# Performance work log

Measured on AMD Instinct MI355X. Metric: run time of the kernel, lower is better.

Reference implementation:

```python
import jax, jax.numpy as jnp
import numpy as np


def setup_inputs() -> dict:
    key = jax.random.key(0)
    ks = jax.random.split(key, 6)
    Q, S, D, C = 128, 512, 768, 64
    return {
        "query_reps": jax.random.normal(ks[0], (Q, D), dtype=jnp.float32),
        "support_reps": jax.random.normal(ks[1], (S, D), dtype=jnp.float32),
        "W1": jax.random.normal(ks[2], (2 * D, 2 * D), dtype=jnp.float32) * 0.02,
        "b1": jnp.zeros((2 * D,), dtype=jnp.float32),
        "W2": jax.random.normal(ks[3], (1, 2 * D), dtype=jnp.float32) * 0.02,
        "b2": jnp.zeros((1,), dtype=jnp.float32),
        "support_labels": jnp.sort(jax.random.randint(ks[4], (S,), 0, C)),
        "query_target_ids": jax.random.randint(ks[5], (Q,), 0, C),
        "num_classes": C,
    }


def reference(query_reps, support_reps, W1, b1, W2, b2,
              support_labels, query_target_ids, num_classes):
    D = query_reps.shape[1]
    # Original: concat_reps = cat([repeat_interleave(q, S), s.repeat(Q)], dim=1)
    # then relu(Linear_2Dx2D(concat)). Equivalent split-weight form avoids the
    # explicit [Q*S, 2D] concat: x @ W1.T = q @ W1[:, :D].T + s @ W1[:, D:].T
    hq = query_reps @ W1[:, :D].T        # [Q, 2D]
    hs = support_reps @ W1[:, D:].T      # [S, 2D]
    h = jax.nn.relu(hq[:, None, :] + hs[None, :, :] + b1)   # [Q, S, 2D]
    scores = jnp.einsum('qsd,d->qs', h, W2[0]) + b2[0]       # [Q, S]
    # aggregate_scores_by_label with support_reduction='score':
    # M one-hot [C, S] row-normalized (p=1) => per-label mean of scores.
    seg = jax.ops.segment_sum(scores.T, support_labels,
                              num_segments=num_classes).T     # [Q, C]
    counts = jax.ops.segment_sum(jnp.ones((support_labels.shape[0],), jnp.float32),
                                 support_labels, num_segments=num_classes)
    agg = seg / jnp.maximum(counts, 1.0)                      # [Q, C]
    logp = jax.nn.log_softmax(agg, axis=1)
    loss = -jnp.mean(jnp.take_along_axis(logp, query_target_ids[:, None], axis=1))
    preds = jnp.argmax(agg, axis=1)
    return (loss, preds == query_target_ids)
```

## Files before the change

### kernel.cpp

```cpp
#include <hip/hip_runtime.h>
#include <math.h>

#define QN 128
#define SN 512
#define DN 768
#define TDN 1536
#define CN 64
#define KSPLIT 4
#define KCH 192

#define HQP_ELEMS (KSPLIT * QN * TDN)
#define HSP_ELEMS (KSPLIT * SN * TDN)
#define ZERO_ELEMS (QN * CN)

typedef short short8 __attribute__((ext_vector_type(8)));
typedef float f32x4 __attribute__((ext_vector_type(4)));

#define LDS_STRIDE 40
#define PLANE (128 * LDS_STRIDE)

__device__ __forceinline__ short bf16_rtn(float x) {
    unsigned u = __float_as_uint(x);
    return (short)((u + 0x7fffu + ((u >> 16) & 1u)) >> 16);
}
__device__ __forceinline__ float bf16_tof(short s) {
    return __uint_as_float(((unsigned)(unsigned short)s) << 16);
}

__global__ __launch_bounds__(256) void gemm_kernel(
    const float* __restrict__ query, const float* __restrict__ support,
    const float* __restrict__ W1, float* __restrict__ hqp, float* __restrict__ hsp,
    float* __restrict__ zbuf, float* __restrict__ out)
{
    const int nt = blockIdx.x;
    const int mt = blockIdx.y;
    const int kz = blockIdx.z;
    const int tid = threadIdx.x;

    if (nt == 0 && kz == 0) {
        int o = (mt * 256 + tid) * 8;
        if (o < ZERO_ELEMS) {
            *(float4*)&zbuf[o]     = make_float4(0.f, 0.f, 0.f, 0.f);
            *(float4*)&zbuf[o + 4] = make_float4(0.f, 0.f, 0.f, 0.f);
        }
        if (mt == 0 && tid == 0) out[0] = 0.0f;
    }

    const float* A;
    float* Cout;
    int M0, Koff;
    if (mt == 0) { A = query;   M0 = 0;              Koff = 0;  Cout = hqp + (size_t)kz * QN * TDN; }
    else         { A = support; M0 = (mt - 1) * 128; Koff = DN; Cout = hsp + (size_t)kz * SN * TDN; }

    __shared__ short lds[2][4][PLANE];

    const int r  = tid >> 1;
    const int kh = (tid & 1) * 16;

    const float* Arow = &A [(size_t)(M0 + r) * DN  + kz * KCH + kh];
    const float* Brow = &W1[(size_t)(nt * 128 + r) * TDN + Koff + kz * KCH + kh];

    f32x4 acc[4][4];
    #pragma unroll
    for (int i = 0; i < 4; ++i)
        #pragma unroll
        for (int j = 0; j < 4; ++j)
            acc[i][j] = (f32x4){0.f, 0.f, 0.f, 0.f};

    auto stage = [&](short* plane, float4 v0, float4 v1, float4 v2, float4 v3) {
        float f[16] = {v0.x,v0.y,v0.z,v0.w, v1.x,v1.y,v1.z,v1.w,
                       v2.x,v2.y,v2.z,v2.w, v3.x,v3.y,v3.z,v3.w};
        short hi[16], lo[16];
        #pragma unroll
        for (int i = 0; i < 16; ++i) {
            hi[i] = bf16_rtn(f[i]);
            lo[i] = bf16_rtn(f[i] - bf16_tof(hi[i]));
        }
        short* dsth = plane + r * LDS_STRIDE + kh;
        #pragma unroll
        for (int i = 0; i < 16; ++i) dsth[i] = hi[i];
        short* dstl = plane + PLANE + r * LDS_STRIDE + kh;
        #pragma unroll
        for (int i = 0; i < 16; ++i) dstl[i] = lo[i];
    };

    {
        float4 a0 = *(const float4*)(Arow),     a1 = *(const float4*)(Arow + 4);
        float4 a2 = *(const float4*)(Arow + 8), a3 = *(const float4*)(Arow + 12);
        float4 b0 = *(const float4*)(Brow),     b1 = *(const float4*)(Brow + 4);
        float4 b2 = *(const float4*)(Brow + 8), b3 = *(const float4*)(Brow + 12);
        stage(lds[0][0], a0, a1, a2, a3);
        stage(lds[0][2], b0, b1, b2, b3);
    }
    __syncthreads();

    const int lane  = tid & 63;
    const int w     = tid >> 6;
    const int lm    = lane & 15;
    const int quad  = lane >> 4;
    const int wrow0 = (w >> 1) * 64;
    const int wcol0 = (w & 1) * 64;

    int buf = 0;
    for (int step = 0; step < 6; ++step) {
        float4 a0, a1, a2, a3, b0, b1, b2, b3;
        if (step < 5) {
            const float* An = Arow + (step + 1) * 32;
            const float* Bn = Brow + (step + 1) * 32;
            a0 = *(const float4*)(An);     a1 = *(const float4*)(An + 4);
            a2 = *(const float4*)(An + 8); a3 = *(const float4*)(An + 12);
            b0 = *(const float4*)(Bn);     b1 = *(const float4*)(Bn + 4);
            b2 = *(const float4*)(Bn + 8); b3 = *(const float4*)(Bn + 12);
        }

        const short* Ah = lds[buf][0];
        const short* Al = lds[buf][1];
        const short* Bh = lds[buf][2];
        const short* Bl = lds[buf][3];

        short8 ah[4], al[4], bh[4], bl[4];
        #pragma unroll
        for (int mi = 0; mi < 4; ++mi) {
            int off = (wrow0 + mi * 16 + lm) * LDS_STRIDE + quad * 8;
            ah[mi] = *(const short8*)&Ah[off];
            al[mi] = *(const short8*)&Al[off];
        }
        #pragma unroll
        for (int ni = 0; ni < 4; ++ni) {
            int off = (wcol0 + ni * 16 + lm) * LDS_STRIDE + quad * 8;
            bh[ni] = *(const short8*)&Bh[off];
            bl[ni] = *(const short8*)&Bl[off];
        }
        #pragma unroll
        for (int mi = 0; mi < 4; ++mi)
            #pragma unroll
            for (int ni = 0; ni < 4; ++ni) {
                acc[mi][ni] = __builtin_amdgcn_mfma_f32_16x16x32_bf16(ah[mi], bh[ni], acc[mi][ni], 0, 0, 0);
                acc[mi][ni] = __builtin_amdgcn_mfma_f32_16x16x32_bf16(ah[mi], bl[ni], acc[mi][ni], 0, 0, 0);
                acc[mi][ni] = __builtin_amdgcn_mfma_f32_16x16x32_bf16(al[mi], bh[ni], acc[mi][ni], 0, 0, 0);
            }

        if (step < 5) {
            int nb = buf ^ 1;
            stage(lds[nb][0], a0, a1, a2, a3);
            stage(lds[nb][2], b0, b1, b2, b3);
            __syncthreads();
            buf = nb;
        }
    }

    #pragma unroll
    for (int mi = 0; mi < 4; ++mi)
        #pragma unroll
        for (int ni = 0; ni < 4; ++ni) {
            int grow = M0 + wrow0 + mi * 16 + quad * 4;
            int gcol = nt * 128 + wcol0 + ni * 16 + lm;
            #pragma unroll
            for (int rr = 0; rr < 4; ++rr)
                Cout[(size_t)(grow + rr) * TDN + gcol] = acc[mi][ni][rr];
        }
}

__global__ __launch_bounds__(256) void score_kernel(
    const float* __restrict__ hqp, const float* __restrict__ hsp,
    const float* __restrict__ b1, const float* __restrict__ W2,
    const int* __restrict__ labels, float* __restrict__ aggbuf)
{
    const int jc = blockIdx.x;
    const int qt = blockIdx.y;
    const int st = blockIdx.z;

    __shared__ float hqT[96][64];
    __shared__ float hsT[96][64];
    __shared__ float w2s[96];
    __shared__ float sc[64][68];
    __shared__ int   lab[64];

    const int tid = threadIdx.x;
    if (tid < 64) lab[tid] = labels[st * 64 + tid];

    #pragma unroll
    for (int l = 0; l < 6; ++l) {
        int idx  = tid + l * 256;
        int row  = idx / 24;
        int quad = idx - row * 24;
        int j    = jc * 96 + quad * 4;
        float4 hv = *(const float4*)&b1[j];
        float4 sv = make_float4(0.f, 0.f, 0.f, 0.f);
        #pragma unroll
        for (int p = 0; p < KSPLIT; ++p) {
            float4 h = *(const float4*)&hqp[(size_t)p * QN * TDN + (size_t)(qt * 64 + row) * TDN + j];
            float4 g = *(const float4*)&hsp[(size_t)p * SN * TDN + (size_t)(st * 64 + row) * TDN + j];
            hv.x += h.x; hv.y += h.y; hv.z += h.z; hv.w += h.w;
            sv.x += g.x; sv.y += g.y; sv.z += g.z; sv.w += g.w;
        }
        hqT[quad*4+0][row] = hv.x; hqT[quad*4+1][row] = hv.y;
        hqT[quad*4+2][row] = hv.z; hqT[quad*4+3][row] = hv.w;
        hsT[quad*4+0][row] = sv.x; hsT[quad*4+1][row] = sv.y;
        hsT[quad*4+2][row] = sv.z; hsT[quad*4+3][row] = sv.w;
    }
    if (tid < 24) {
        float4 w = *(const float4*)&W2[jc * 96 + tid * 4];
        w2s[tid*4+0] = w.x; w2s[tid*4+1] = w.y;
        w2s[tid*4+2] = w.z; w2s[tid*4+3] = w.w;
    }
    __syncthreads();

    const int tx = tid & 15;
    const int ty = tid >> 4;
    float acc[4][4];
    #pragma unroll
    for (int i = 0; i < 4; ++i)
        #pragma unroll
        for (int j = 0; j < 4; ++j) acc[i][j] = 0.0f;

    #pragma unroll 4
    for (int jj = 0; jj < 96; ++jj) {
        float4 a4 = *(const float4*)&hqT[jj][ty * 4];
        float4 b4 = *(const float4*)&hsT[jj][tx * 4];
        float w = w2s[jj];
        float a[4] = {a4.x, a4.y, a4.z, a4.w};
        float b[4] = {b4.x, b4.y, b4.z, b4.w};
        #pragma unroll
        for (int i = 0; i < 4; ++i)
            #pragma unroll
            for (int j = 0; j < 4; ++j)
                acc[i][j] += w * fmaxf(a[i] + b[j], 0.0f);
    }

    #pragma unroll
    for (int i = 0; i < 4; ++i)
        *(float4*)&sc[ty * 4 + i][tx * 4] =
            make_float4(acc[i][0], acc[i][1], acc[i][2], acc[i][3]);
    __syncthreads();

    {
        int row = tid >> 2;
        int seg = tid & 3;
        float* aggrow = aggbuf + (size_t)(qt * 64 + row) * CN;
        int   runc = lab[seg * 16];
        float runv = 0.0f;
        #pragma unroll
        for (int k = 0; k < 16; ++k) {
            int s = seg * 16 + k;
            int c = lab[s];
            if (c != runc) { atomicAdd(&aggrow[runc], runv); runv = 0.0f; runc = c; }
            runv += sc[row][s];
        }
        atomicAdd(&aggrow[runc], runv);
    }
}

__global__ __launch_bounds__(256) void finale_kernel(
    const float* __restrict__ aggbuf, const int* __restrict__ labels,
    const int* __restrict__ tgt, float* __restrict__ out)
{
    __shared__ float cnt[CN];
    const int tid = threadIdx.x;
    if (tid < CN) cnt[tid] = 0.0f;
    __syncthreads();
    atomicAdd(&cnt[labels[tid]],       1.0f);
    atomicAdd(&cnt[labels[tid + 256]], 1.0f);
    __syncthreads();

    const int lane = tid & 63;
    const int q    = blockIdx.x * 4 + (tid >> 6);

    float v = aggbuf[(size_t)q * CN + lane] / fmaxf(cnt[lane], 1.0f);
    float av = v; int am = lane;
    #pragma unroll
    for (int off = 1; off < 64; off <<= 1) {
        float ov = __shfl_xor(av, off);
        int   oi = __shfl_xor(am, off);
        if (ov > av || (ov == av && oi < am)) { av = ov; am = oi; }
    }
    float m = av;
    float e = expf(v - m);
    #pragma unroll
    for (int off = 1; off < 64; off <<= 1)
        e += __shfl_xor(e, off);
    int t = tgt[q];
    float vt = __shfl(v, t, 64);
    if (lane == 0) {
        out[1 + q] = (am == t) ? 1.0f : 0.0f;
        atomicAdd(&out[0], -(vt - m - logf(e)) / (float)QN);
    }
}

extern "C" void kernel_launch(void* const* d_in, const int* in_sizes, int n_in,
                              void* d_out, int out_size, void* d_ws, size_t ws_size,
                              hipStream_t stream) {
    const float* query   = (const float*)d_in[0];
    const float* support = (const float*)d_in[1];
    const float* W1      = (const float*)d_in[2];
    const float* b1      = (const float*)d_in[3];
    const float* W2      = (const float*)d_in[4];
    const int* labels = (const int*)d_in[6];
    const int* tgt    = (const int*)d_in[7];

    float* ws     = (float*)d_ws;
    float* hqp    = ws;
    float* hsp    = hqp + HQP_ELEMS;
    float* aggbuf = hsp + HSP_ELEMS;
    float* out    = (float*)d_out;

    hipLaunchKernelGGL(gemm_kernel, dim3(12, 5, 4), dim3(256), 0, stream,
                       query, support, W1, hqp, hsp, aggbuf, out);
    hipLaunchKernelGGL(score_kernel, dim3(16, 2, 8), dim3(256), 0, stream,
                       hqp, hsp, b1, W2, labels, aggbuf);
    hipLaunchKernelGGL(finale_kernel, dim3(32), dim3(256), 0, stream,
                       aggbuf, labels, tgt, out);
}
```

Baseline: 119.0 us.

## Fuse GEMM, scoring and finale into one cooperative kernel with grid syncs

Replaces the three kernel launches with a single cooperative kernel of 256 blocks. Blocks 0-239 run the split-K GEMM, block 240 zeroes the aggregation buffer, and the score stage and finale follow after grid-wide barriers. The finale now runs in one block, with one thread per query doing a serial loop over classes, and the loss is reduced without global atomics. The goal is to remove launch gaps between kernels, at the cost of grid-sync overhead, a serialized single-block finale and LDS shared through a union.

Measured after the change: 202.7 us. 1.7x slower.

```diff
diff --git a/kernel.cpp b/kernel.cpp
--- a/kernel.cpp
+++ b/kernel.cpp
@@ -1,5 +1,8 @@
 #include <hip/hip_runtime.h>
+#include <hip/hip_cooperative_groups.h>
 #include <math.h>
+
+namespace cg = cooperative_groups;
 
 #define QN 128
 #define SN 512
@@ -11,7 +14,6 @@
 
 #define HQP_ELEMS (KSPLIT * QN * TDN)
 #define HSP_ELEMS (KSPLIT * SN * TDN)
-#define ZERO_ELEMS (QN * CN)
 
 typedef short short8 __attribute__((ext_vector_type(8)));
 typedef float f32x4 __attribute__((ext_vector_type(4)));
@@ -27,263 +29,280 @@
     return __uint_as_float(((unsigned)(unsigned short)s) << 16);
 }
 
-__global__ __launch_bounds__(256) void gemm_kernel(
+__global__ __launch_bounds__(256) void mega_kernel(
     const float* __restrict__ query, const float* __restrict__ support,
-    const float* __restrict__ W1, float* __restrict__ hqp, float* __restrict__ hsp,
-    float* __restrict__ zbuf, float* __restrict__ out)
+    const float* __restrict__ W1, const float* __restrict__ b1,
+    const float* __restrict__ W2, const int* __restrict__ labels,
+    const int* __restrict__ tgt, float* __restrict__ hqp,
+    float* __restrict__ hsp, float* __restrict__ aggbuf,
+    float* __restrict__ out)
 {
-    const int nt = blockIdx.x;
-    const int mt = blockIdx.y;
-    const int kz = blockIdx.z;
+    const int bid = blockIdx.x;
     const int tid = threadIdx.x;
 
-    if (nt == 0 && kz == 0) {
-        int o = (mt * 256 + tid) * 8;
-        if (o < ZERO_ELEMS) {
-            *(float4*)&zbuf[o]     = make_float4(0.f, 0.f, 0.f, 0.f);
-            *(float4*)&zbuf[o + 4] = make_float4(0.f, 0.f, 0.f, 0.f);
-        }
-        if (mt == 0 && tid == 0) out[0] = 0.0f;
+    __shared__ union {
+        short g[2][4][PLANE];
+        struct {
+            float hqT[96][64];
+            float hsT[96][64];
+            float w2s[96];
+            float sc[64][68];
+            int   lab[64];
+            float cnt[64];
+            float red[4];
+        } s;
+    } sh;
+
+    cg::grid_group grid = cg::this_grid();
+
+    if (bid >= 240) {
+        if (bid == 240) {
+            #pragma unroll
+            for (int i = 0; i < 8; ++i)
+                *(float4*)&aggbuf[(tid * 8 + i * 2048)] = make_float4(0.f,0.f,0.f,0.f);
+        }
+    } else {
+        const int nt = bid % 12;
+        const int mt = (bid / 12) % 5;
+        const int kz = bid / 60;
+
+        const float* A;
+        float* Cout;
+        int M0, Koff;
+        if (mt == 0) { A = query;   M0 = 0;              Koff = 0;  Cout = hqp + (size_t)kz * QN * TDN; }
+        else         { A = support; M0 = (mt - 1) * 128; Koff = DN; Cout = hsp + (size_t)kz * SN * TDN; }
+
+        const int r  = tid >> 1;
+        const int kh = (tid & 1) * 16;
+
+        const float* Arow = &A [(size_t)(M0 + r) * DN  + kz * KCH + kh];
+        const float* Brow = &W1[(size_t)(nt * 128 + r) * TDN + Koff + kz * KCH + kh];
+
+        f32x4 acc[4][4];
+        #pragma unroll
+        for (int i = 0; i < 4; ++i)
+            #pragma unroll
+            for (int j = 0; j < 4; ++j)
+                acc[i][j] = (f32x4){0.f, 0.f, 0.f, 0.f};
+
+        auto stage = [&](short* plane, float4 v0, float4 v1, float4 v2, float4 v3) {
+            float f[16] = {v0.x,v0.y,v0.z,v0.w, v1.x,v1.y,v1.z,v1.w,
+                           v2.x,v2.y,v2.z,v2.w, v3.x,v3.y,v3.z,v3.w};
+            short hi[16], lo[16];
+            #pragma unroll
+            for (int i = 0; i < 16; ++i) {
+                hi[i] = bf16_rtn(f[i]);
+                lo[i] = bf16_rtn(f[i] - bf16_tof(hi[i]));
+            }
+            short* dsth = plane + r * LDS_STRIDE + kh;
+            #pragma unroll
+            for (int i = 0; i < 16; ++i) dsth[i] = hi[i];
+            short* dstl = plane + PLANE + r * LDS_STRIDE + kh;
+            #pragma unroll
+            for (int i = 0; i < 16; ++i) dstl[i] = lo[i];
+        };
+
+        {
+            float4 a0 = *(const float4*)(Arow),     a1 = *(const float4*)(Arow + 4);
+            float4 a2 = *(const float4*)(Arow + 8), a3 = *(const float4*)(Arow + 12);
+            float4 b0 = *(const float4*)(Brow),     b1 = *(const float4*)(Brow + 4);
+            float4 b2 = *(const float4*)(Brow + 8), b3 = *(const float4*)(Brow + 12);
+            stage(sh.g[0][0], a0, a1, a2, a3);
+            stage(sh.g[0][2], b0, b1, b2, b3);
+        }
+        __syncthreads();
+
+        const int lane  = tid & 63;
+        const int w     = tid >> 6;
+        const int lm    = lane & 15;
+        const int quad  = lane >> 4;
+        const int wrow0 = (w >> 1) * 64;
+        const int wcol0 = (w & 1) * 64;
+
+        int buf = 0;
+        for (int step = 0; step < 6; ++step) {
+            float4 a0, a1, a2, a3, b0, b1, b2, b3;
+            if (step < 5) {
+                const float* An = Arow + (step + 1) * 32;
+                const float* Bn = Brow + (step + 1) * 32;
+                a0 = *(const float4*)(An);     a1 = *(const float4*)(An + 4);
+                a2 = *(const float4*)(An + 8); a3 = *(const float4*)(An + 12);
+                b0 = *(const float4*)(Bn);     b1 = *(const float4*)(Bn + 4);
+                b2 = *(const float4*)(Bn + 8); b3 = *(const float4*)(Bn + 12);
+            }
+
+            const short* Ah = sh.g[buf][0];
+            const short* Al = sh.g[buf][1];
+            const short* Bh = sh.g[buf][2];
+            const short* Bl = sh.g[buf][3];
+
+            short8 ah[4], al[4], bh[4], bl[4];
+            #pragma unroll
+            for (int mi = 0; mi < 4; ++mi) {
+                int off = (wrow0 + mi * 16 + lm) * LDS_STRIDE + quad * 8;
+                ah[mi] = *(const short8*)&Ah[off];
+                al[mi] = *(const short8*)&Al[off];
+            }
+            #pragma unroll
+            for (int ni = 0; ni < 4; ++ni) {
+                int off = (wcol0 + ni * 16 + lm) * LDS_STRIDE + quad * 8;
+                bh[ni] = *(const short8*)&Bh[off];
+                bl[ni] = *(const short8*)&Bl[off];
+            }
+            #pragma unroll
+            for (int mi = 0; mi < 4; ++mi)
+                #pragma unroll
+                for (int ni = 0; ni < 4; ++ni) {
+                    acc[mi][ni] = __builtin_amdgcn_mfma_f32_16x16x32_bf16(ah[mi], bh[ni], acc[mi][ni], 0, 0, 0);
+                    acc[mi][ni] = __builtin_amdgcn_mfma_f32_16x16x32_bf16(ah[mi], bl[ni], acc[mi][ni], 0, 0, 0);
+                    acc[mi][ni] = __builtin_amdgcn_mfma_f32_16x16x32_bf16(al[mi], bh[ni], acc[mi][ni], 0, 0, 0);
+                }
+
+            if (step < 5) {
+                int nb = buf ^ 1;
+                stage(sh.g[nb][0], a0, a1, a2, a3);
+                stage(sh.g[nb][2], b0, b1, b2, b3);
+                __syncthreads();
+                buf = nb;
+            }
+        }
+
+        #pragma unroll
+        for (int mi = 0; mi < 4; ++mi)
+            #pragma unroll
+            for (int ni = 0; ni < 4; ++ni) {
+                int grow = M0 + wrow0 + mi * 16 + quad * 4;
+                int gcol = nt * 128 + wcol0 + ni * 16 + lm;
+                #pragma unroll
+                for (int rr = 0; rr < 4; ++rr)
+                    Cout[(size_t)(grow + rr) * TDN + gcol] = acc[mi][ni][rr];
+            }
     }
 
-    const float* A;
-    float* Cout;
-    int M0, Koff;
-    if (mt == 0) { A = query;   M0 = 0;              Koff = 0;  Cout = hqp + (size_t)kz * QN * TDN; }
-    else         { A = support; M0 = (mt - 1) * 128; Koff = DN; Cout = hsp + (size_t)kz * SN * TDN; }
-
-    __shared__ short lds[2][4][PLANE];
-
-    const int r  = tid >> 1;
-    const int kh = (tid & 1) * 16;
-
-    const float* Arow = &A [(size_t)(M0 + r) * DN  + kz * KCH + kh];
-    const float* Brow = &W1[(size_t)(nt * 128 + r) * TDN + Koff + kz * KCH + kh];
-
-    f32x4 acc[4][4];
-    #pragma unroll
-    for (int i = 0; i < 4; ++i)
-        #pragma unroll
-        for (int j = 0; j < 4; ++j)
-            acc[i][j] = (f32x4){0.f, 0.f, 0.f, 0.f};
-
-    auto stage = [&](short* plane, float4 v0, float4 v1, float4 v2, float4 v3) {
-        float f[16] = {v0.x,v0.y,v0.z,v0.w, v1.x,v1.y,v1.z,v1.w,
-                       v2.x,v2.y,v2.z,v2.w, v3.x,v3.y,v3.z,v3.w};
-        short hi[16], lo[16];
-        #pragma unroll
-        for (int i = 0; i < 16; ++i) {
-            hi[i] = bf16_rtn(f[i]);
-            lo[i] = bf16_rtn(f[i] - bf16_tof(hi[i]));
-        }
-        short* dsth = plane + r * LDS_STRIDE + kh;
-        #pragma unroll
-        for (int i = 0; i < 16; ++i) dsth[i] = hi[i];
-        short* dstl = plane + PLANE + r * LDS_STRIDE + kh;
-        #pragma unroll
-        for (int i = 0; i < 16; ++i) dstl[i] = lo[i];
-    };
+    grid.sync();
 
     {
-        float4 a0 = *(const float4*)(Arow),     a1 = *(const float4*)(Arow + 4);
-        float4 a2 = *(const float4*)(Arow + 8), a3 = *(const float4*)(Arow + 12);
-        float4 b0 = *(const float4*)(Brow),     b1 = *(const float4*)(Brow + 4);
-        float4 b2 = *(const float4*)(Brow + 8), b3 = *(const float4*)(Brow + 12);
-        stage(lds[0][0], a0, a1, a2, a3);
-        stage(lds[0][2], b0, b1, b2, b3);
+        const int jc = bid & 15;
+        const int qt = (bid >> 4) & 1;
+        const int st = bid >> 5;
+
+        if (tid < 64) sh.s.lab[tid] = labels[st * 64 + tid];
+
+        #pragma unroll
+        for (int l = 0; l < 6; ++l) {
+            int idx  = tid + l * 256;
+            int row  = idx / 24;
+            int quad = idx - row * 24;
+            int j    = jc * 96 + quad * 4;
+            float4 hv = *(const float4*)&b1[j];
+            float4 sv = make_float4(0.f, 0.f, 0.f, 0.f);
+            #pragma unroll
+            for (int p = 0; p < KSPLIT; ++p) {
+                float4 h = *(const float4*)&hqp[(size_t)p * QN * TDN + (size_t)(qt * 64 + row) * TDN + j];
+                float4 g = *(const float4*)&hsp[(size_t)p * SN * TDN + (size_t)(st * 64 + row) * TDN + j];
+                hv.x += h.x; hv.y += h.y; hv.z += h.z; hv.w += h.w;
+                sv.x += g.x; sv.y += g.y; sv.z += g.z; sv.w += g.w;
+            }
+            sh.s.hqT[quad*4+0][row] = hv.x; sh.s.hqT[quad*4+1][row] = hv.y;
+            sh.s.hqT[quad*4+2][row] = hv.z; sh.s.hqT[quad*4+3][row] = hv.w;
+            sh.s.hsT[quad*4+0][row] = sv.x; sh.s.hsT[quad*4+1][row] = sv.y;
+            sh.s.hsT[quad*4+2][row] = sv.z; sh.s.hsT[quad*4+3][row] = sv.w;
+        }
+        if (tid < 24) {
+            float4 wv = *(const float4*)&W2[jc * 96 + tid * 4];
+            sh.s.w2s[tid*4+0] = wv.x; sh.s.w2s[tid*4+1] = wv.y;
+            sh.s.w2s[tid*4+2] = wv.z; sh.s.w2s[tid*4+3] = wv.w;
+        }
+        __syncthreads();
+
+        const int tx = tid & 15;
+        const int ty = tid >> 4;
+        float acc[4][4];
+        #pragma unroll
+        for (int i = 0; i < 4; ++i)
+            #pragma unroll
+            for (int j = 0; j < 4; ++j) acc[i][j] = 0.0f;
+
+        #pragma unroll 4
+        for (int jj = 0; jj < 96; ++jj) {
+            float4 a4 = *(const float4*)&sh.s.hqT[jj][ty * 4];
+            float4 b4 = *(const float4*)&sh.s.hsT[jj][tx * 4];
+            float wv = sh.s.w2s[jj];
+            float a[4] = {a4.x, a4.y, a4.z, a4.w};
+            float b[4] = {b4.x, b4.y, b4.z, b4.w};
+            #pragma unroll
+            for (int i = 0; i < 4; ++i)
+                #pragma unroll
+                for (int j = 0; j < 4; ++j)
+                    acc[i][j] += wv * fmaxf(a[i] + b[j], 0.0f);
+        }
+
+        #pragma unroll
+        for (int i = 0; i < 4; ++i)
+            *(float4*)&sh.s.sc[ty * 4 + i][tx * 4] =
+                make_float4(acc[i][0], acc[i][1], acc[i][2], acc[i][3]);
+        __syncthreads();
+
+        {
+            int row = tid >> 2;
+            int seg = tid & 3;
+            float* aggrow = aggbuf + (size_t)(qt * 64 + row) * CN;
+            int   runc = sh.s.lab[seg * 16];
+            float runv = 0.0f;
+            #pragma unroll
+            for (int k = 0; k < 16; ++k) {
+                int s = seg * 16 + k;
+                int c = sh.s.lab[s];
+                if (c != runc) { atomicAdd(&aggrow[runc], runv); runv = 0.0f; runc = c; }
+                runv += sh.s.sc[row][s];
+            }
+            atomicAdd(&aggrow[runc], runv);
+        }
     }
-    __syncthreads();
-
-    const int lane  = tid & 63;
-    const int w     = tid >> 6;
-    const int lm    = lane & 15;
-    const int quad  = lane >> 4;
-    const int wrow0 = (w >> 1) * 64;
-    const int wcol0 = (w & 1) * 64;
-
-    int buf = 0;
-    for (int step = 0; step < 6; ++step) {
-        float4 a0, a1, a2, a3, b0, b1, b2, b3;
-        if (step < 5) {
-            const float* An = Arow + (step + 1) * 32;
-            const float* Bn = Brow + (step + 1) * 32;
-            a0 = *(const float4*)(An);     a1 = *(const float4*)(An + 4);
-            a2 = *(const float4*)(An + 8); a3 = *(const float4*)(An + 12);
-            b0 = *(const float4*)(Bn);     b1 = *(const float4*)(Bn + 4);
-            b2 = *(const float4*)(Bn + 8); b3 = *(const float4*)(Bn + 12);
-        }
-
-        const short* Ah = lds[buf][0];
-        const short* Al = lds[buf][1];
-        const short* Bh = lds[buf][2];
-        const short* Bl = lds[buf][3];
-
-        short8 ah[4], al[4], bh[4], bl[4];
-        #pragma unroll
-        for (int mi = 0; mi < 4; ++mi) {
-            int off = (wrow0 + mi * 16 + lm) * LDS_STRIDE + quad * 8;
-            ah[mi] = *(const short8*)&Ah[off];
-            al[mi] = *(const short8*)&Al[off];
-        }
-        #pragma unroll
-        for (int ni = 0; ni < 4; ++ni) {
-            int off = (wcol0 + ni * 16 + lm) * LDS_STRIDE + quad * 8;
-            bh[ni] = *(const short8*)&Bh[off];
-            bl[ni] = *(const short8*)&Bl[off];
-        }
-        #pragma unroll
-        for (int mi = 0; mi < 4; ++mi)
-            #pragma unroll
-            for (int ni = 0; ni < 4; ++ni) {
-                acc[mi][ni] = __builtin_amdgcn_mfma_f32_16x16x32_bf16(ah[mi], bh[ni], acc[mi][ni], 0, 0, 0);
-                acc[mi][ni] = __builtin_amdgcn_mfma_f32_16x16x32_bf16(ah[mi], bl[ni], acc[mi][ni], 0, 0, 0);
-                acc[mi][ni] = __builtin_amdgcn_mfma_f32_16x16x32_bf16(al[mi], bh[ni], acc[mi][ni], 0, 0, 0);
-            }
-
-        if (step < 5) {
-            int nb = buf ^ 1;
-            stage(lds[nb][0], a0, a1, a2, a3);
-            stage(lds[nb][2], b0, b1, b2, b3);
-            __syncthreads();
-            buf = nb;
-        }
-    }
-
-    #pragma unroll
-    for (int mi = 0; mi < 4; ++mi)
-        #pragma unroll
-        for (int ni = 0; ni < 4; ++ni) {
-            int grow = M0 + wrow0 + mi * 16 + quad * 4;
-            int gcol = nt * 128 + wcol0 + ni * 16 + lm;
-            #pragma unroll
-            for (int rr = 0; rr < 4; ++rr)
-                Cout[(size_t)(grow + rr) * TDN + gcol] = acc[mi][ni][rr];
-        }
-}
-
-__global__ __launch_bounds__(256) void score_kernel(
-    const float* __restrict__ hqp, const float* __restrict__ hsp,
-    const float* __restrict__ b1, const float* __restrict__ W2,
-    const int* __restrict__ labels, float* __restrict__ aggbuf)
-{
-    const int jc = blockIdx.x;
-    const int qt = blockIdx.y;
-    const int st = blockIdx.z;
-
-    __shared__ float hqT[96][64];
-    __shared__ float hsT[96][64];
-    __shared__ float w2s[96];
-    __shared__ float sc[64][68];
-    __shared__ int   lab[64];
-
-    const int tid = threadIdx.x;
-    if (tid < 64) lab[tid] = labels[st * 64 + tid];
-
-    #pragma unroll
-    for (int l = 0; l < 6; ++l) {
-        int idx  = tid + l * 256;
-        int row  = idx / 24;
-        int quad = idx - row * 24;
-        int j    = jc * 96 + quad * 4;
-        float4 hv = *(const float4*)&b1[j];
-        float4 sv = make_float4(0.f, 0.f, 0.f, 0.f);
-        #pragma unroll
-        for (int p = 0; p < KSPLIT; ++p) {
-            float4 h = *(const float4*)&hqp[(size_t)p * QN * TDN + (size_t)(qt * 64 + row) * TDN + j];
-            float4 g = *(const float4*)&hsp[(size_t)p * SN * TDN + (size_t)(st * 64 + row) * TDN + j];
-            hv.x += h.x; hv.y += h.y; hv.z += h.z; hv.w += h.w;
-            sv.x += g.x; sv.y += g.y; sv.z += g.z; sv.w += g.w;
-        }
-        hqT[quad*4+0][row] = hv.x; hqT[quad*4+1][row] = hv.y;
-        hqT[quad*4+2][row] = hv.z; hqT[quad*4+3][row] = hv.w;
-        hsT[quad*4+0][row] = sv.x; hsT[quad*4+1][row] = sv.y;
-        hsT[quad*4+2][row] = sv.z; hsT[quad*4+3][row] = sv.w;
-    }
-    if (tid < 24) {
-        float4 w = *(const float4*)&W2[jc * 96 + tid * 4];
-        w2s[tid*4+0] = w.x; w2s[tid*4+1] = w.y;
-        w2s[tid*4+2] = w.z; w2s[tid*4+3] = w.w;
-    }
-    __syncthreads();
-
-    const int tx = tid & 15;
-    const int ty = tid >> 4;
-    float acc[4][4];
-    #pragma unroll
-    for (int i = 0; i < 4; ++i)
-        #pragma unroll
-        for (int j = 0; j < 4; ++j) acc[i][j] = 0.0f;
-
-    #pragma unroll 4
-    for (int jj = 0; jj < 96; ++jj) {
-        float4 a4 = *(const float4*)&hqT[jj][ty * 4];
-        float4 b4 = *(const float4*)&hsT[jj][tx * 4];
-        float w = w2s[jj];
-        float a[4] = {a4.x, a4.y, a4.z, a4.w};
-        float b[4] = {b4.x, b4.y, b4.z, b4.w};
-        #pragma unroll
-        for (int i = 0; i < 4; ++i)
-            #pragma unroll
-            for (int j = 0; j < 4; ++j)
-                acc[i][j] += w * fmaxf(a[i] + b[j], 0.0f);
-    }
-
-    #pragma unroll
-    for (int i = 0; i < 4; ++i)
-        *(float4*)&sc[ty * 4 + i][tx * 4] =
-            make_float4(acc[i][0], acc[i][1], acc[i][2], acc[i][3]);
-    __syncthreads();
-
-    {
-        int row = tid >> 2;
-        int seg = tid & 3;
-        float* aggrow = aggbuf + (size_t)(qt * 64 + row) * CN;
-        int   runc = lab[seg * 16];
-        float runv = 0.0f;
-        #pragma unroll
-        for (int k = 0; k < 16; ++k) {
-            int s = seg * 16 + k;
-            int c = lab[s];
-            if (c != runc) { atomicAdd(&aggrow[runc], runv); runv = 0.0f; runc = c; }
-            runv += sc[row][s];
-        }
-        atomicAdd(&aggrow[runc], runv);
-    }
-}
-
-__global__ __launch_bounds__(256) void finale_kernel(
-    const float* __restrict__ aggbuf, const int* __restrict__ labels,
-    const int* __restrict__ tgt, float* __restrict__ out)
-{
-    __shared__ float cnt[CN];
-    const int tid = threadIdx.x;
-    if (tid < CN) cnt[tid] = 0.0f;
-    __syncthreads();
-    atomicAdd(&cnt[labels[tid]],       1.0f);
-    atomicAdd(&cnt[labels[tid + 256]], 1.0f);
-    __syncthreads();
-
-    const int lane = tid & 63;
-    const int q    = blockIdx.x * 4 + (tid >> 6);
-
-    float v = aggbuf[(size_t)q * CN + lane] / fmaxf(cnt[lane], 1.0f);
-    float av = v; int am = lane;
-    #pragma unroll
-    for (int off = 1; off < 64; off <<= 1) {
-        float ov = __shfl_xor(av, off);
-        int   oi = __shfl_xor(am, off);
-        if (ov > av || (ov == av && oi < am)) { av = ov; am = oi; }
-    }
-    float m = av;
-    float e = expf(v - m);
-    #pragma unroll
-    for (int off = 1; off < 64; off <<= 1)
-        e += __shfl_xor(e, off);
-    int t = tgt[q];
-    float vt = __shfl(v, t, 64);
-    if (lane == 0) {
-        out[1 + q] = (am == t) ? 1.0f : 0.0f;
-        atomicAdd(&out[0], -(vt - m - logf(e)) / (float)QN);
+
+    grid.sync();
+
+    if (bid == 0) {
+        if (tid < CN) sh.s.cnt[tid] = 0.0f;
+        __syncthreads();
+        atomicAdd(&sh.s.cnt[labels[tid]],       1.0f);
+        atomicAdd(&sh.s.cnt[labels[tid + 256]], 1.0f);
+        __syncthreads();
+
+        float lossv = 0.0f;
+        if (tid < QN) {
+            const int q = tid;
+            const float* rowp = aggbuf + (size_t)q * CN;
+            float v[CN];
+            #pragma unroll
+            for (int c4 = 0; c4 < 16; ++c4) {
+                float4 t4 = *(const float4*)&rowp[c4 * 4];
+                v[c4*4+0] = t4.x; v[c4*4+1] = t4.y;
+                v[c4*4+2] = t4.z; v[c4*4+3] = t4.w;
+            }
+            const int t = tgt[q];
+            float vt = 0.0f;
+            float best = -1e30f; int bi = 0;
+            #pragma unroll
+            for (int c = 0; c < CN; ++c) {
+                v[c] /= fmaxf(sh.s.cnt[c], 1.0f);
+                if (c == t) vt = v[c];
+                if (v[c] > best) { best = v[c]; bi = c; }
+            }
+            float e = 0.0f;
+            #pragma unroll
+            for (int c = 0; c < CN; ++c)
+                e += expf(v[c] - best);
+            out[1 + q] = (bi == t) ? 1.0f : 0.0f;
+            lossv = -(vt - best - logf(e));
+        }
+        #pragma unroll
+        for (int off = 1; off < 64; off <<= 1)
+            lossv += __shfl_xor(lossv, off);
+        if ((tid & 63) == 0) sh.s.red[tid >> 6] = lossv;
+        __syncthreads();
+        if (tid == 0)
+            out[0] = (sh.s.red[0] + sh.s.red[1]) / (float)QN;
     }
 }
 
@@ -304,10 +323,9 @@
     float* aggbuf = hsp + HSP_ELEMS;
     float* out    = (float*)d_out;
 
-    hipLaunchKernelGGL(gemm_kernel, dim3(12, 5, 4), dim3(256), 0, stream,
-                       query, support, W1, hqp, hsp, aggbuf, out);
-    hipLaunchKernelGGL(score_kernel, dim3(16, 2, 8), dim3(256), 0, stream,
-                       hqp, hsp, b1, W2, labels, aggbuf);
-    hipLaunchKernelGGL(finale_kernel, dim3(32), dim3(256), 0, stream,
-                       aggbuf, labels, tgt, out);
+    void* args[] = { (void*)&query, (void*)&support, (void*)&W1, (void*)&b1,
+                     (void*)&W2, (void*)&labels, (void*)&tgt,
+                     (void*)&hqp, (void*)&hsp, (void*)&aggbuf, (void*)&out };
+    hipLaunchCooperativeKernel((const void*)mega_kernel,
+                               dim3(256), dim3(256), args, 0, stream);
 }
```

## Halve GEMM split-K and fuse finale into score kernel via last-block counter

Applied to the files above, without the earlier changes.

Reduces the GEMM split-K factor from 4 to 2, doubling the K chunk per block, which halves the partial-sum traffic that the score kernel must read and sum. Removes the separate finale kernel by having the last score block, detected through an atomic completion counter, compute the log-softmax loss and argmax accuracy. This saves one launch and the partial-buffer bandwidth, but the GEMM grid shrinks to 120 blocks with longer serial K loops, and the finale now runs on a single block.

After: 143.6 us. 1.21x slower.

```diff
diff --git a/kernel.cpp b/kernel.cpp
--- a/kernel.cpp
+++ b/kernel.cpp
@@ -6,8 +6,8 @@
 #define DN 768
 #define TDN 1536
 #define CN 64
-#define KSPLIT 4
-#define KCH 192
+#define KSPLIT 2
+#define KCH 384
 
 #define HQP_ELEMS (KSPLIT * QN * TDN)
 #define HSP_ELEMS (KSPLIT * SN * TDN)
@@ -30,7 +30,7 @@
 __global__ __launch_bounds__(256) void gemm_kernel(
     const float* __restrict__ query, const float* __restrict__ support,
     const float* __restrict__ W1, float* __restrict__ hqp, float* __restrict__ hsp,
-    float* __restrict__ zbuf, float* __restrict__ out)
+    float* __restrict__ zbuf, int* __restrict__ donecnt)
 {
     const int nt = blockIdx.x;
     const int mt = blockIdx.y;
@@ -43,7 +43,7 @@
             *(float4*)&zbuf[o]     = make_float4(0.f, 0.f, 0.f, 0.f);
             *(float4*)&zbuf[o + 4] = make_float4(0.f, 0.f, 0.f, 0.f);
         }
-        if (mt == 0 && tid == 0) out[0] = 0.0f;
+        if (mt == 0 && tid == 0) *donecnt = 0;
     }
 
     const float* A;
@@ -102,9 +102,9 @@
     const int wcol0 = (w & 1) * 64;
 
     int buf = 0;
-    for (int step = 0; step < 6; ++step) {
+    for (int step = 0; step < 12; ++step) {
         float4 a0, a1, a2, a3, b0, b1, b2, b3;
-        if (step < 5) {
+        if (step < 11) {
             const float* An = Arow + (step + 1) * 32;
             const float* Bn = Brow + (step + 1) * 32;
             a0 = *(const float4*)(An);     a1 = *(const float4*)(An + 4);
@@ -140,7 +140,7 @@
                 acc[mi][ni] = __builtin_amdgcn_mfma_f32_16x16x32_bf16(al[mi], bh[ni], acc[mi][ni], 0, 0, 0);
             }
 
-        if (step < 5) {
+        if (step < 11) {
             int nb = buf ^ 1;
             stage(lds[nb][0], a0, a1, a2, a3);
             stage(lds[nb][2], b0, b1, b2, b3);
@@ -164,7 +164,9 @@
 __global__ __launch_bounds__(256) void score_kernel(
     const float* __restrict__ hqp, const float* __restrict__ hsp,
     const float* __restrict__ b1, const float* __restrict__ W2,
-    const int* __restrict__ labels, float* __restrict__ aggbuf)
+    const int* __restrict__ labels, const int* __restrict__ tgt,
+    float* __restrict__ aggbuf, int* __restrict__ donecnt,
+    float* __restrict__ out)
 {
     const int jc = blockIdx.x;
     const int qt = blockIdx.y;
@@ -175,6 +177,9 @@
     __shared__ float w2s[96];
     __shared__ float sc[64][68];
     __shared__ int   lab[64];
+    __shared__ float cnt[CN];
+    __shared__ float red[2];
+    __shared__ int   isLast;
 
     const int tid = threadIdx.x;
     if (tid < 64) lab[tid] = labels[st * 64 + tid];
@@ -200,9 +205,9 @@
         hsT[quad*4+2][row] = sv.z; hsT[quad*4+3][row] = sv.w;
     }
     if (tid < 24) {
-        float4 w = *(const float4*)&W2[jc * 96 + tid * 4];
-        w2s[tid*4+0] = w.x; w2s[tid*4+1] = w.y;
-        w2s[tid*4+2] = w.z; w2s[tid*4+3] = w.w;
+        float4 wv = *(const float4*)&W2[jc * 96 + tid * 4];
+        w2s[tid*4+0] = wv.x; w2s[tid*4+1] = wv.y;
+        w2s[tid*4+2] = wv.z; w2s[tid*4+3] = wv.w;
     }
     __syncthreads();
 
@@ -218,14 +223,14 @@
     for (int jj = 0; jj < 96; ++jj) {
         float4 a4 = *(const float4*)&hqT[jj][ty * 4];
         float4 b4 = *(const float4*)&hsT[jj][tx * 4];
-        float w = w2s[jj];
+        float wv = w2s[jj];
         float a[4] = {a4.x, a4.y, a4.z, a4.w};
         float b[4] = {b4.x, b4.y, b4.z, b4.w};
         #pragma unroll
         for (int i = 0; i < 4; ++i)
             #pragma unroll
             for (int j = 0; j < 4; ++j)
-                acc[i][j] += w * fmaxf(a[i] + b[j], 0.0f);
+                acc[i][j] += wv * fmaxf(a[i] + b[j], 0.0f);
     }
 
     #pragma unroll
@@ -249,42 +254,54 @@
         }
         atomicAdd(&aggrow[runc], runv);
     }
-}
-
-__global__ __launch_bounds__(256) void finale_kernel(
-    const float* __restrict__ aggbuf, const int* __restrict__ labels,
-    const int* __restrict__ tgt, float* __restrict__ out)
-{
-    __shared__ float cnt[CN];
-    const int tid = threadIdx.x;
+
+    __syncthreads();
+    if (tid == 0) {
+        __threadfence();
+        isLast = (atomicAdd(donecnt, 1) == 255);
+    }
+    __syncthreads();
+    if (!isLast) return;
+    __threadfence();
+
     if (tid < CN) cnt[tid] = 0.0f;
     __syncthreads();
     atomicAdd(&cnt[labels[tid]],       1.0f);
     atomicAdd(&cnt[labels[tid + 256]], 1.0f);
     __syncthreads();
 
-    const int lane = tid & 63;
-    const int q    = blockIdx.x * 4 + (tid >> 6);
-
-    float v = aggbuf[(size_t)q * CN + lane] / fmaxf(cnt[lane], 1.0f);
-    float av = v; int am = lane;
-    #pragma unroll
-    for (int off = 1; off < 64; off <<= 1) {
-        float ov = __shfl_xor(av, off);
-        int   oi = __shfl_xor(am, off);
-        if (ov > av || (ov == av && oi < am)) { av = ov; am = oi; }
-    }
-    float m = av;
-    float e = expf(v - m);
+    float lossv = 0.0f;
+    if (tid < QN) {
+        const int q = tid;
+        const float* rowp = aggbuf + (size_t)q * CN;
+        const int t = tgt[q];
+        float best = -1e30f, vt = 0.0f;
+        int bi = 0;
+        #pragma unroll
+        for (int c = 0; c < CN; ++c) {
+            float v = __hip_atomic_load(&rowp[c], __ATOMIC_RELAXED,
+                                        __HIP_MEMORY_SCOPE_AGENT)
+                      / fmaxf(cnt[c], 1.0f);
+            if (v > best) { best = v; bi = c; }
+            if (c == t) vt = v;
+        }
+        float e = 0.0f;
+        #pragma unroll
+        for (int c = 0; c < CN; ++c) {
+            float v = __hip_atomic_load(&rowp[c], __ATOMIC_RELAXED,
+                                        __HIP_MEMORY_SCOPE_AGENT)
+                      / fmaxf(cnt[c], 1.0f);
+            e += expf(v - best);
+        }
+        out[1 + q] = (bi == t) ? 1.0f : 0.0f;
+        lossv = -(vt - best - logf(e));
+    }
     #pragma unroll
     for (int off = 1; off < 64; off <<= 1)
-        e += __shfl_xor(e, off);
-    int t = tgt[q];
-    float vt = __shfl(v, t, 64);
-    if (lane == 0) {
-        out[1 + q] = (am == t) ? 1.0f : 0.0f;
-        atomicAdd(&out[0], -(vt - m - logf(e)) / (float)QN);
-    }
+        lossv += __shfl_xor(lossv, off);
+    if ((tid & 63) == 0) red[tid >> 6] = lossv;
+    __syncthreads();
+    if (tid == 0) out[0] = (red[0] + red[1]) / (float)QN;
 }
 
 extern "C" void kernel_launch(void* const* d_in, const int* in_sizes, int n_in,
@@ -298,16 +315,15 @@
     const int* labels = (const int*)d_in[6];
     const int* tgt    = (const int*)d_in[7];
 
-    float* ws     = (float*)d_ws;
-    float* hqp    = ws;
-    float* hsp    = hqp + HQP_ELEMS;
-    float* aggbuf = hsp + HSP_ELEMS;
-    float* out    = (float*)d_out;
-
-    hipLaunchKernelGGL(gemm_kernel, dim3(12, 5, 4), dim3(256), 0, stream,
-                       query, support, W1, hqp, hsp, aggbuf, out);
+    float* ws      = (float*)d_ws;
+    float* hqp     = ws;
+    float* hsp     = hqp + HQP_ELEMS;
+    float* aggbuf  = hsp + HSP_ELEMS;
+    int*   donecnt = (int*)(aggbuf + QN * CN);
+    float* out     = (float*)d_out;
+
+    hipLaunchKernelGGL(gemm_kernel, dim3(12, 5, 2), dim3(256), 0, stream,
+                       query, support, W1, hqp, hsp, aggbuf, donecnt);
     hipLaunchKernelGGL(score_kernel, dim3(16, 2, 8), dim3(256), 0, stream,
-                       hqp, hsp, b1, W2, labels, aggbuf);
-    hipLaunchKernelGGL(finale_kernel, dim3(32), dim3(256), 0, stream,
-                       aggbuf, labels, tgt, out);
-}
+                       hqp, hsp, b1, W2, labels, tgt, aggbuf, donecnt, out);
+}
```
